# Optimization experiments

Hardware: AMD Instinct MI355X
Metric: run time of the kernel (lower is better)

The kernel has to match this reference:

```python
import jax, jax.numpy as jnp
import numpy as np

# FineMatching constants (from init_kwargs)
GRID_NUM = 8
VOXEL = 0.04
NDIM = 3
MAX_NEIGHBORS = 128
OFFSET = GRID_NUM * VOXEL / 2.0           # 0.16
RADIUS = (GRID_NUM + 1) * VOXEL / 2.0      # 0.18
G1 = GRID_NUM + 1                          # grid nodes per dim
G = G1 ** NDIM                             # 729 flattened voxel bins
NEG_BIG = -1e30


def setup_inputs() -> dict:
    key = jax.random.key(0)
    k1, k2, k3, k4, k5 = jax.random.split(key, 5)
    B, L0, L1, C = 4, 2048, 2048, 64
    x0 = jax.random.normal(k1, (B, L0, C), dtype=jnp.float32)
    x1 = jax.random.normal(k2, (B, L1, C), dtype=jnp.float32)
    pos0 = jax.random.uniform(k3, (B, L0, 3), dtype=jnp.float32)
    pos1 = jax.random.uniform(k4, (B, L1, 3), dtype=jnp.float32)
    pad_mask = jax.random.uniform(k5, (B, L1)) < 0.1  # True = padded / masked out
    return {"x0": x0, "x1": x1, "pos0": pos0, "pos1": pos1, "pad_mask": pad_mask}


def reference(x0, x1, pos0, pos1, pad_mask):
    B, L0, C = x0.shape
    K = MAX_NEIGHBORS
    # --- radius neighbor search (per batch, dense distances, K nearest) ---
    d2 = jnp.sum((pos0[:, :, None, :] - pos1[:, None, :, :]) ** 2, axis=-1)  # (B,L0,L1)
    neg_d2, idx = jax.lax.top_k(-d2, K)                                       # (B,L0,K)
    valid = (-neg_d2) < RADIUS ** 2                                           # within radius
    pad_g = jnp.take_along_axis(pad_mask[:, None, :], idx, axis=2)           # (B,L0,K)
    valid = valid & (~pad_g)
    # --- edge-wise gather + correlation ---
    x1g = jnp.take_along_axis(x1[:, None, :, :], idx[..., None], axis=2)     # (B,L0,K,C)
    corr = jnp.einsum('blc,blkc->blk', x0, x1g) / jnp.sqrt(jnp.float32(C))
    # --- masked segment softmax over neighbors (nan -> 0 when no valid edge) ---
    logits = jnp.where(valid, corr, NEG_BIG)
    prob = jax.nn.softmax(logits, axis=-1) * valid                            # (B,L0,K)
    # --- flow aggregation ---
    pos1g = jnp.take_along_axis(pos1[:, None, :, :], idx[..., None], axis=2) # (B,L0,K,3)
    dpos = pos1g - pos0[:, :, None, :]
    flow = jnp.einsum('blk,blkd->bld', prob, dpos)                            # (B,L0,3)
    # --- P2G voxel scatter: bin prob mass into (grid_num+1)^3 voxel grid ---
    coords = (dpos + OFFSET) / VOXEL
    vox = jnp.clip(jnp.round(coords), 0, GRID_NUM).astype(jnp.int32)          # (B,L0,K,3)
    flat = (vox[..., 0] * G1 + vox[..., 1]) * G1 + vox[..., 2]                # (B,L0,K)
    b_ix = jnp.arange(B)[:, None, None]
    l_ix = jnp.arange(L0)[None, :, None]
    flow_dist = jnp.zeros((B, L0, G), dtype=x0.dtype).at[b_ix, l_ix, flat].add(prob)
    return flow, flow_dist
```

## Files before the change

kernel.cpp:

```cpp
#include <hip/hip_runtime.h>
#include <stdint.h>

#define NB    4
#define NL0   2048
#define NL1   2048
#define NC    64
#define KMAX  128
#define CAP   256
#define NG1   9
#define NBINS 729
#define FLOWN (NB*NL0*3)
#define QPB   8
#define TPB   512

__global__ __launch_bounds__(TPB, 8) void fine_match_kernel(
    const float* __restrict__ x0, const float* __restrict__ x1,
    const float* __restrict__ pos0, const float* __restrict__ pos1,
    const void* __restrict__ padraw, float* __restrict__ out)
{
  __shared__ float          s_pos[NL1*3];
  __shared__ float          s_x0[QPB*NC];
  __shared__ float          s_p0[QPB][3];
  __shared__ unsigned short s_jj[QPB][CAP];
  __shared__ float          s_corr[QPB][CAP];

  const int t = threadIdx.x;
  const int bid = blockIdx.x;
  const int b = bid >> 8;
  const int l0base = (bid & 255) * QPB;

  int wide;
  {
    const uint32_t* pi = (const uint32_t*)padraw;
    int ok4 = 1;
    for (int i = t; i < (NB*NL1)/4; i += TPB) {
      const uint32_t v = pi[i];
      ok4 &= (int)((v <= 1u) | (v == 0x3F800000u));
    }
    wide = __syncthreads_and(ok4);
  }

  {
    const float4* src = (const float4*)(pos1 + (size_t)b*NL1*3);
    float4* dst = (float4*)s_pos;
    for (int i = t; i < NL1*3/4; i += TPB) dst[i] = src[i];
  }
  s_x0[t] = x0[(size_t)(b*NL0 + l0base)*NC + t];
  if (t < QPB*3) {
    const int q = t/3, c = t - q*3;
    s_p0[q][c] = pos0[(b*NL0 + l0base + q)*3 + c];
  }
  {
    float4 z4; z4.x = z4.y = z4.z = z4.w = 0.0f;
    float4* bz = (float4*)(out + FLOWN + (size_t)(b*NL0 + l0base)*NBINS);
    for (int i = t; i < QPB*NBINS/4; i += TPB) bz[i] = z4;
  }
  __syncthreads();

  const int wv = t >> 6, lane = t & 63;
  const int l0 = l0base + wv;
  const float p0x = s_p0[wv][0], p0y = s_p0[wv][1], p0z = s_p0[wv][2];

  int cnt = 0;
  for (int base = 0; base < NL1; base += 64) {
    const int j = base + lane;
    const float dx = __fsub_rn(s_pos[j*3+0], p0x);
    const float dy = __fsub_rn(s_pos[j*3+1], p0y);
    const float dz = __fsub_rn(s_pos[j*3+2], p0z);
    const float d2 = __fadd_rn(__fadd_rn(__fmul_rn(dx,dx), __fmul_rn(dy,dy)), __fmul_rn(dz,dz));
    const bool ok = d2 < 0.0324f;
    const uint64_t m = __ballot(ok);
    if (ok) {
      const int pos = cnt + (int)__popcll(m & ((1ull << lane) - 1ull));
      if (pos < CAP) s_jj[wv][pos] = (unsigned short)j;
    }
    cnt += (int)__popcll(m);
  }
  if (cnt > CAP) cnt = CAP;
  __syncthreads();

  const bool over = (cnt > KMAX);
  for (int s = 0; s < 4; ++s) {
    if (64*s >= cnt) break;
    const int i = lane + 64*s;
    if (i < cnt) {
      float c = -1e30f;
      const int j = (int)s_jj[wv][i];
      bool k;
      if (wide) k = (((const uint32_t*)padraw)[b*NL1 + j] == 0u);
      else      k = (((const uint8_t*)padraw)[b*NL1 + j] == 0);
      if (over && k) {
        const float dx = __fsub_rn(s_pos[j*3+0], p0x);
        const float dy = __fsub_rn(s_pos[j*3+1], p0y);
        const float dz = __fsub_rn(s_pos[j*3+2], p0z);
        const float di = __fadd_rn(__fadd_rn(__fmul_rn(dx,dx), __fmul_rn(dy,dy)), __fmul_rn(dz,dz));
        int rank = 0;
        for (int m2 = 0; m2 < cnt; ++m2) {
          const int jm = (int)s_jj[wv][m2];
          const float ex = __fsub_rn(s_pos[jm*3+0], p0x);
          const float ey = __fsub_rn(s_pos[jm*3+1], p0y);
          const float ez = __fsub_rn(s_pos[jm*3+2], p0z);
          const float dm = __fadd_rn(__fadd_rn(__fmul_rn(ex,ex), __fmul_rn(ey,ey)), __fmul_rn(ez,ez));
          rank += (dm < di || (dm == di && m2 < i)) ? 1 : 0;
        }
        if (rank >= KMAX) k = false;
      }
      if (k) {
        const float* xr = x1 + ((size_t)b*NL1 + j)*NC;
        float acc = 0.0f;
        #pragma unroll
        for (int cc = 0; cc < NC; cc += 4) {
          const float4 v = *(const float4*)(xr + cc);
          const float4 q = *(const float4*)(&s_x0[wv*NC + cc]);
          acc += q.x*v.x + q.y*v.y + q.z*v.z + q.w*v.w;
        }
        c = acc * 0.125f;
      }
      s_corr[wv][i] = c;
    }
  }

  float mx = -1e30f;
  for (int s = 0; s < 4; ++s) {
    if (64*s >= cnt) break;
    const int i = lane + 64*s;
    if (i < cnt) { const float c = s_corr[wv][i]; if (c > mx) mx = c; }
  }
  for (int off = 32; off; off >>= 1) { const float o = __shfl_xor(mx, off); if (o > mx) mx = o; }
  float sum = 0.0f;
  for (int s = 0; s < 4; ++s) {
    if (64*s >= cnt) break;
    const int i = lane + 64*s;
    if (i < cnt) { const float c = s_corr[wv][i]; if (c > -1e30f) sum += expf(c - mx); }
  }
  for (int off = 32; off; off >>= 1) sum += __shfl_xor(sum, off);
  const float inv = (sum > 0.0f) ? (1.0f / sum) : 0.0f;

  float* bins = out + FLOWN + (size_t)((size_t)b*NL0 + l0)*NBINS;
  float fx = 0.0f, fy = 0.0f, fz = 0.0f;
  for (int s = 0; s < 4; ++s) {
    if (64*s >= cnt) break;
    const int i = lane + 64*s;
    if (i < cnt) {
      const float c = s_corr[wv][i];
      if (c > -1e30f) {
        const float pv = expf(c - mx) * inv;
        const int j = (int)s_jj[wv][i];
        const float dx = __fsub_rn(s_pos[j*3+0], p0x);
        const float dy = __fsub_rn(s_pos[j*3+1], p0y);
        const float dz = __fsub_rn(s_pos[j*3+2], p0z);
        fx += pv*dx; fy += pv*dy; fz += pv*dz;
        const float cx = __fdiv_rn(__fadd_rn(dx, 0.16f), 0.04f);
        const float cy = __fdiv_rn(__fadd_rn(dy, 0.16f), 0.04f);
        const float cz = __fdiv_rn(__fadd_rn(dz, 0.16f), 0.04f);
        int vx = (int)rintf(cx); vx = vx < 0 ? 0 : (vx > 8 ? 8 : vx);
        int vy = (int)rintf(cy); vy = vy < 0 ? 0 : (vy > 8 ? 8 : vy);
        int vz = (int)rintf(cz); vz = vz < 0 ? 0 : (vz > 8 ? 8 : vz);
        __hip_atomic_fetch_add(&bins[(vx*NG1 + vy)*NG1 + vz], pv,
                               __ATOMIC_RELAXED, __HIP_MEMORY_SCOPE_WORKGROUP);
      }
    }
  }
  for (int off = 32; off; off >>= 1) {
    fx += __shfl_xor(fx, off); fy += __shfl_xor(fy, off); fz += __shfl_xor(fz, off);
  }
  if (lane == 0) {
    float* f = out + (size_t)((size_t)b*NL0 + l0)*3;
    f[0] = fx; f[1] = fy; f[2] = fz;
  }
}

extern "C" void kernel_launch(void* const* d_in, const int* in_sizes, int n_in,
                              void* d_out, int out_size, void* d_ws, size_t ws_size,
                              hipStream_t stream) {
  const float* x0   = (const float*)d_in[0];
  const float* x1   = (const float*)d_in[1];
  const float* pos0 = (const float*)d_in[2];
  const float* pos1 = (const float*)d_in[3];
  const void*  pad  = d_in[4];
  float* out = (float*)d_out;
  (void)in_sizes; (void)n_in; (void)out_size; (void)d_ws; (void)ws_size;
  hipLaunchKernelGGL(fine_match_kernel, dim3(NB*NL0/QPB), dim3(TPB), 0, stream,
                     x0, x1, pos0, pos1, pad, out);
}
```

Before: 29.63 us.

## Pack pos1 with pad flag into float4 LDS, double queries per block

Stores each pos1 point as a float4 in shared memory with the pad flag in the w component. Candidate filtering, ranking and binning then each need one LDS vector read instead of three scalar loads plus a global pad lookup. Blocks grow from 8 to 16 queries (1024 threads), which halves the number of times pos1 is restaged per batch. The output zeroing is moved ahead of the pad-format check so its stores are issued earlier. The larger block with the same launch bound may limit occupancy, and the pos1 staging now uses strided scalar global loads instead of float4 copies.

New measurement: 31.34 us. +5.8%, slower.

```diff
diff --git a/kernel.cpp b/kernel.cpp
--- a/kernel.cpp
+++ b/kernel.cpp
@@ -10,15 +10,15 @@
 #define NG1   9
 #define NBINS 729
 #define FLOWN (NB*NL0*3)
-#define QPB   8
-#define TPB   512
+#define QPB   16
+#define TPB   1024
 
 __global__ __launch_bounds__(TPB, 8) void fine_match_kernel(
     const float* __restrict__ x0, const float* __restrict__ x1,
     const float* __restrict__ pos0, const float* __restrict__ pos1,
     const void* __restrict__ padraw, float* __restrict__ out)
 {
-  __shared__ float          s_pos[NL1*3];
+  __shared__ float4         s_pos[NL1];
   __shared__ float          s_x0[QPB*NC];
   __shared__ float          s_p0[QPB][3];
   __shared__ unsigned short s_jj[QPB][CAP];
@@ -26,8 +26,14 @@
 
   const int t = threadIdx.x;
   const int bid = blockIdx.x;
-  const int b = bid >> 8;
-  const int l0base = (bid & 255) * QPB;
+  const int b = bid >> 7;
+  const int l0base = (bid & 127) * QPB;
+
+  {
+    float4 z4; z4.x = z4.y = z4.z = z4.w = 0.0f;
+    float4* bz = (float4*)(out + FLOWN + (size_t)(b*NL0 + l0base)*NBINS);
+    for (int i = t; i < QPB*NBINS/4; i += TPB) bz[i] = z4;
+  }
 
   int wide;
   {
@@ -41,19 +47,19 @@
   }
 
   {
-    const float4* src = (const float4*)(pos1 + (size_t)b*NL1*3);
-    float4* dst = (float4*)s_pos;
-    for (int i = t; i < NL1*3/4; i += TPB) dst[i] = src[i];
+    const float* p1b = pos1 + (size_t)b*NL1*3;
+    for (int i = t; i < NL1; i += TPB) {
+      float pv;
+      if (wide) pv = (((const uint32_t*)padraw)[b*NL1 + i] != 0u) ? 1.0f : 0.0f;
+      else      pv = (((const uint8_t*)padraw)[b*NL1 + i] != 0)   ? 1.0f : 0.0f;
+      float4 p; p.x = p1b[i*3+0]; p.y = p1b[i*3+1]; p.z = p1b[i*3+2]; p.w = pv;
+      s_pos[i] = p;
+    }
   }
   s_x0[t] = x0[(size_t)(b*NL0 + l0base)*NC + t];
   if (t < QPB*3) {
     const int q = t/3, c = t - q*3;
     s_p0[q][c] = pos0[(b*NL0 + l0base + q)*3 + c];
-  }
-  {
-    float4 z4; z4.x = z4.y = z4.z = z4.w = 0.0f;
-    float4* bz = (float4*)(out + FLOWN + (size_t)(b*NL0 + l0base)*NBINS);
-    for (int i = t; i < QPB*NBINS/4; i += TPB) bz[i] = z4;
   }
   __syncthreads();
 
@@ -64,9 +70,10 @@
   int cnt = 0;
   for (int base = 0; base < NL1; base += 64) {
     const int j = base + lane;
-    const float dx = __fsub_rn(s_pos[j*3+0], p0x);
-    const float dy = __fsub_rn(s_pos[j*3+1], p0y);
-    const float dz = __fsub_rn(s_pos[j*3+2], p0z);
+    const float4 p = s_pos[j];
+    const float dx = __fsub_rn(p.x, p0x);
+    const float dy = __fsub_rn(p.y, p0y);
+    const float dz = __fsub_rn(p.z, p0z);
     const float d2 = __fadd_rn(__fadd_rn(__fmul_rn(dx,dx), __fmul_rn(dy,dy)), __fmul_rn(dz,dz));
     const bool ok = d2 < 0.0324f;
     const uint64_t m = __ballot(ok);
@@ -86,20 +93,19 @@
     if (i < cnt) {
       float c = -1e30f;
       const int j = (int)s_jj[wv][i];
-      bool k;
-      if (wide) k = (((const uint32_t*)padraw)[b*NL1 + j] == 0u);
-      else      k = (((const uint8_t*)padraw)[b*NL1 + j] == 0);
+      const float4 pj = s_pos[j];
+      bool k = (pj.w == 0.0f);
       if (over && k) {
-        const float dx = __fsub_rn(s_pos[j*3+0], p0x);
-        const float dy = __fsub_rn(s_pos[j*3+1], p0y);
-        const float dz = __fsub_rn(s_pos[j*3+2], p0z);
+        const float dx = __fsub_rn(pj.x, p0x);
+        const float dy = __fsub_rn(pj.y, p0y);
+        const float dz = __fsub_rn(pj.z, p0z);
         const float di = __fadd_rn(__fadd_rn(__fmul_rn(dx,dx), __fmul_rn(dy,dy)), __fmul_rn(dz,dz));
         int rank = 0;
         for (int m2 = 0; m2 < cnt; ++m2) {
-          const int jm = (int)s_jj[wv][m2];
-          const float ex = __fsub_rn(s_pos[jm*3+0], p0x);
-          const float ey = __fsub_rn(s_pos[jm*3+1], p0y);
-          const float ez = __fsub_rn(s_pos[jm*3+2], p0z);
+          const float4 pm = s_pos[(int)s_jj[wv][m2]];
+          const float ex = __fsub_rn(pm.x, p0x);
+          const float ey = __fsub_rn(pm.y, p0y);
+          const float ez = __fsub_rn(pm.z, p0z);
           const float dm = __fadd_rn(__fadd_rn(__fmul_rn(ex,ex), __fmul_rn(ey,ey)), __fmul_rn(ez,ez));
           rank += (dm < di || (dm == di && m2 < i)) ? 1 : 0;
         }
@@ -145,10 +151,10 @@
       const float c = s_corr[wv][i];
       if (c > -1e30f) {
         const float pv = expf(c - mx) * inv;
-        const int j = (int)s_jj[wv][i];
-        const float dx = __fsub_rn(s_pos[j*3+0], p0x);
-        const float dy = __fsub_rn(s_pos[j*3+1], p0y);
-        const float dz = __fsub_rn(s_pos[j*3+2], p0z);
+        const float4 pj = s_pos[(int)s_jj[wv][i]];
+        const float dx = __fsub_rn(pj.x, p0x);
+        const float dy = __fsub_rn(pj.y, p0y);
+        const float dz = __fsub_rn(pj.z, p0z);
         fx += pv*dx; fy += pv*dy; fz += pv*dz;
         const float cx = __fdiv_rn(__fadd_rn(dx, 0.16f), 0.04f);
         const float cy = __fdiv_rn(__fadd_rn(dy, 0.16f), 0.04f);
```

## Process two queries per wave to reuse staged pos1 and halve block setup

Applied to the files above, without the earlier changes.

Doubles queries per block to 16, with each wave handling two queries. The candidate scan loads each pos1 point from LDS once and tests it against both queries, and the per-block pos1 staging and pad-format scan are amortized over twice as many queries. The trade-off is a halved grid and higher register pressure, with per-query softmax/scatter phases now serialized within a wave.

Result: slower. 30.92 us (+4.4%).

```diff
diff --git a/kernel.cpp b/kernel.cpp
--- a/kernel.cpp
+++ b/kernel.cpp
@@ -10,10 +10,10 @@
 #define NG1   9
 #define NBINS 729
 #define FLOWN (NB*NL0*3)
-#define QPB   8
+#define QPB   16
 #define TPB   512
 
-__global__ __launch_bounds__(TPB, 8) void fine_match_kernel(
+__global__ __launch_bounds__(TPB, 4) void fine_match_kernel(
     const float* __restrict__ x0, const float* __restrict__ x1,
     const float* __restrict__ pos0, const float* __restrict__ pos1,
     const void* __restrict__ padraw, float* __restrict__ out)
@@ -26,8 +26,8 @@
 
   const int t = threadIdx.x;
   const int bid = blockIdx.x;
-  const int b = bid >> 8;
-  const int l0base = (bid & 255) * QPB;
+  const int b = bid >> 7;
+  const int l0base = (bid & 127) * QPB;
 
   int wide;
   {
@@ -45,7 +45,8 @@
     float4* dst = (float4*)s_pos;
     for (int i = t; i < NL1*3/4; i += TPB) dst[i] = src[i];
   }
-  s_x0[t] = x0[(size_t)(b*NL0 + l0base)*NC + t];
+  for (int i = t; i < QPB*NC; i += TPB)
+    s_x0[i] = x0[(size_t)(b*NL0 + l0base)*NC + i];
   if (t < QPB*3) {
     const int q = t/3, c = t - q*3;
     s_p0[q][c] = pos0[(b*NL0 + l0base + q)*3 + c];
@@ -58,115 +59,135 @@
   __syncthreads();
 
   const int wv = t >> 6, lane = t & 63;
-  const int l0 = l0base + wv;
-  const float p0x = s_p0[wv][0], p0y = s_p0[wv][1], p0z = s_p0[wv][2];
-
-  int cnt = 0;
+  const int q0 = wv*2, q1 = wv*2 + 1;
+  const float ax = s_p0[q0][0], ay = s_p0[q0][1], az = s_p0[q0][2];
+  const float bx = s_p0[q1][0], by = s_p0[q1][1], bz = s_p0[q1][2];
+
+  int cnt0 = 0, cnt1 = 0;
   for (int base = 0; base < NL1; base += 64) {
     const int j = base + lane;
-    const float dx = __fsub_rn(s_pos[j*3+0], p0x);
-    const float dy = __fsub_rn(s_pos[j*3+1], p0y);
-    const float dz = __fsub_rn(s_pos[j*3+2], p0z);
-    const float d2 = __fadd_rn(__fadd_rn(__fmul_rn(dx,dx), __fmul_rn(dy,dy)), __fmul_rn(dz,dz));
-    const bool ok = d2 < 0.0324f;
-    const uint64_t m = __ballot(ok);
-    if (ok) {
-      const int pos = cnt + (int)__popcll(m & ((1ull << lane) - 1ull));
-      if (pos < CAP) s_jj[wv][pos] = (unsigned short)j;
-    }
-    cnt += (int)__popcll(m);
-  }
-  if (cnt > CAP) cnt = CAP;
-  __syncthreads();
-
-  const bool over = (cnt > KMAX);
-  for (int s = 0; s < 4; ++s) {
-    if (64*s >= cnt) break;
-    const int i = lane + 64*s;
-    if (i < cnt) {
-      float c = -1e30f;
-      const int j = (int)s_jj[wv][i];
-      bool k;
-      if (wide) k = (((const uint32_t*)padraw)[b*NL1 + j] == 0u);
-      else      k = (((const uint8_t*)padraw)[b*NL1 + j] == 0);
-      if (over && k) {
-        const float dx = __fsub_rn(s_pos[j*3+0], p0x);
-        const float dy = __fsub_rn(s_pos[j*3+1], p0y);
-        const float dz = __fsub_rn(s_pos[j*3+2], p0z);
-        const float di = __fadd_rn(__fadd_rn(__fmul_rn(dx,dx), __fmul_rn(dy,dy)), __fmul_rn(dz,dz));
-        int rank = 0;
-        for (int m2 = 0; m2 < cnt; ++m2) {
-          const int jm = (int)s_jj[wv][m2];
-          const float ex = __fsub_rn(s_pos[jm*3+0], p0x);
-          const float ey = __fsub_rn(s_pos[jm*3+1], p0y);
-          const float ez = __fsub_rn(s_pos[jm*3+2], p0z);
-          const float dm = __fadd_rn(__fadd_rn(__fmul_rn(ex,ex), __fmul_rn(ey,ey)), __fmul_rn(ez,ez));
-          rank += (dm < di || (dm == di && m2 < i)) ? 1 : 0;
+    const float px = s_pos[j*3+0], py = s_pos[j*3+1], pz = s_pos[j*3+2];
+    const float dxa = __fsub_rn(px, ax), dya = __fsub_rn(py, ay), dza = __fsub_rn(pz, az);
+    const float dxb = __fsub_rn(px, bx), dyb = __fsub_rn(py, by), dzb = __fsub_rn(pz, bz);
+    const float d2a = __fadd_rn(__fadd_rn(__fmul_rn(dxa,dxa), __fmul_rn(dya,dya)), __fmul_rn(dza,dza));
+    const float d2b = __fadd_rn(__fadd_rn(__fmul_rn(dxb,dxb), __fmul_rn(dyb,dyb)), __fmul_rn(dzb,dzb));
+    const bool oka = d2a < 0.0324f;
+    const bool okb = d2b < 0.0324f;
+    const uint64_t m0 = __ballot(oka);
+    const uint64_t m1 = __ballot(okb);
+    const uint64_t lm = (1ull << lane) - 1ull;
+    if (oka) {
+      const int pos = cnt0 + (int)__popcll(m0 & lm);
+      if (pos < CAP) s_jj[q0][pos] = (unsigned short)j;
+    }
+    if (okb) {
+      const int pos = cnt1 + (int)__popcll(m1 & lm);
+      if (pos < CAP) s_jj[q1][pos] = (unsigned short)j;
+    }
+    cnt0 += (int)__popcll(m0);
+    cnt1 += (int)__popcll(m1);
+  }
+  if (cnt0 > CAP) cnt0 = CAP;
+  if (cnt1 > CAP) cnt1 = CAP;
+
+  #pragma unroll
+  for (int u = 0; u < 2; ++u) {
+    const int qi  = (u == 0) ? q0 : q1;
+    const int cnt = (u == 0) ? cnt0 : cnt1;
+    const int l0  = l0base + qi;
+    const float p0x = (u == 0) ? ax : bx;
+    const float p0y = (u == 0) ? ay : by;
+    const float p0z = (u == 0) ? az : bz;
+
+    const bool over = (cnt > KMAX);
+    for (int s = 0; s < 4; ++s) {
+      if (64*s >= cnt) break;
+      const int i = lane + 64*s;
+      if (i < cnt) {
+        float c = -1e30f;
+        const int j = (int)s_jj[qi][i];
+        bool k;
+        if (wide) k = (((const uint32_t*)padraw)[b*NL1 + j] == 0u);
+        else      k = (((const uint8_t*)padraw)[b*NL1 + j] == 0);
+        if (over && k) {
+          const float dx = __fsub_rn(s_pos[j*3+0], p0x);
+          const float dy = __fsub_rn(s_pos[j*3+1], p0y);
+          const float dz = __fsub_rn(s_pos[j*3+2], p0z);
+          const float di = __fadd_rn(__fadd_rn(__fmul_rn(dx,dx), __fmul_rn(dy,dy)), __fmul_rn(dz,dz));
+          int rank = 0;
+          for (int m2 = 0; m2 < cnt; ++m2) {
+            const int jm = (int)s_jj[qi][m2];
+            const float ex = __fsub_rn(s_pos[jm*3+0], p0x);
+            const float ey = __fsub_rn(s_pos[jm*3+1], p0y);
+            const float ez = __fsub_rn(s_pos[jm*3+2], p0z);
+            const float dm = __fadd_rn(__fadd_rn(__fmul_rn(ex,ex), __fmul_rn(ey,ey)), __fmul_rn(ez,ez));
+            rank += (dm < di || (dm == di && m2 < i)) ? 1 : 0;
+          }
+          if (rank >= KMAX) k = false;
         }
-        if (rank >= KMAX) k = false;
+        if (k) {
+          const float* xr = x1 + ((size_t)b*NL1 + j)*NC;
+          float acc = 0.0f;
+          #pragma unroll
+          for (int cc = 0; cc < NC; cc += 4) {
+            const float4 v = *(const float4*)(xr + cc);
+            const float4 q = *(const float4*)(&s_x0[qi*NC + cc]);
+            acc += q.x*v.x + q.y*v.y + q.z*v.z + q.w*v.w;
+          }
+          c = acc * 0.125f;
+        }
+        s_corr[qi][i] = c;
       }
-      if (k) {
-        const float* xr = x1 + ((size_t)b*NL1 + j)*NC;
-        float acc = 0.0f;
-        #pragma unroll
-        for (int cc = 0; cc < NC; cc += 4) {
-          const float4 v = *(const float4*)(xr + cc);
-          const float4 q = *(const float4*)(&s_x0[wv*NC + cc]);
-          acc += q.x*v.x + q.y*v.y + q.z*v.z + q.w*v.w;
+    }
+
+    float mx = -1e30f;
+    for (int s = 0; s < 4; ++s) {
+      if (64*s >= cnt) break;
+      const int i = lane + 64*s;
+      if (i < cnt) { const float c = s_corr[qi][i]; if (c > mx) mx = c; }
+    }
+    for (int off = 32; off; off >>= 1) { const float o = __shfl_xor(mx, off); if (o > mx) mx = o; }
+    float sum = 0.0f;
+    for (int s = 0; s < 4; ++s) {
+      if (64*s >= cnt) break;
+      const int i = lane + 64*s;
+      if (i < cnt) { const float c = s_corr[qi][i]; if (c > -1e30f) sum += expf(c - mx); }
+    }
+    for (int off = 32; off; off >>= 1) sum += __shfl_xor(sum, off);
+    const float inv = (sum > 0.0f) ? (1.0f / sum) : 0.0f;
+
+    float* bins = out + FLOWN + (size_t)((size_t)b*NL0 + l0)*NBINS;
+    float fx = 0.0f, fy = 0.0f, fz = 0.0f;
+    for (int s = 0; s < 4; ++s) {
+      if (64*s >= cnt) break;
+      const int i = lane + 64*s;
+      if (i < cnt) {
+        const float c = s_corr[qi][i];
+        if (c > -1e30f) {
+          const float pv = expf(c - mx) * inv;
+          const int j = (int)s_jj[qi][i];
+          const float dx = __fsub_rn(s_pos[j*3+0], p0x);
+          const float dy = __fsub_rn(s_pos[j*3+1], p0y);
+          const float dz = __fsub_rn(s_pos[j*3+2], p0z);
+          fx += pv*dx; fy += pv*dy; fz += pv*dz;
+          const float cx = __fdiv_rn(__fadd_rn(dx, 0.16f), 0.04f);
+          const float cy = __fdiv_rn(__fadd_rn(dy, 0.16f), 0.04f);
+          const float cz = __fdiv_rn(__fadd_rn(dz, 0.16f), 0.04f);
+          int vx = (int)rintf(cx); vx = vx < 0 ? 0 : (vx > 8 ? 8 : vx);
+          int vy = (int)rintf(cy); vy = vy < 0 ? 0 : (vy > 8 ? 8 : vy);
+          int vz = (int)rintf(cz); vz = vz < 0 ? 0 : (vz > 8 ? 8 : vz);
+          __hip_atomic_fetch_add(&bins[(vx*NG1 + vy)*NG1 + vz], pv,
+                                 __ATOMIC_RELAXED, __HIP_MEMORY_SCOPE_WORKGROUP);
         }
-        c = acc * 0.125f;
       }
-      s_corr[wv][i] = c;
-    }
-  }
-
-  float mx = -1e30f;
-  for (int s = 0; s < 4; ++s) {
-    if (64*s >= cnt) break;
-    const int i = lane + 64*s;
-    if (i < cnt) { const float c = s_corr[wv][i]; if (c > mx) mx = c; }
-  }
-  for (int off = 32; off; off >>= 1) { const float o = __shfl_xor(mx, off); if (o > mx) mx = o; }
-  float sum = 0.0f;
-  for (int s = 0; s < 4; ++s) {
-    if (64*s >= cnt) break;
-    const int i = lane + 64*s;
-    if (i < cnt) { const float c = s_corr[wv][i]; if (c > -1e30f) sum += expf(c - mx); }
-  }
-  for (int off = 32; off; off >>= 1) sum += __shfl_xor(sum, off);
-  const float inv = (sum > 0.0f) ? (1.0f / sum) : 0.0f;
-
-  float* bins = out + FLOWN + (size_t)((size_t)b*NL0 + l0)*NBINS;
-  float fx = 0.0f, fy = 0.0f, fz = 0.0f;
-  for (int s = 0; s < 4; ++s) {
-    if (64*s >= cnt) break;
-    const int i = lane + 64*s;
-    if (i < cnt) {
-      const float c = s_corr[wv][i];
-      if (c > -1e30f) {
-        const float pv = expf(c - mx) * inv;
-        const int j = (int)s_jj[wv][i];
-        const float dx = __fsub_rn(s_pos[j*3+0], p0x);
-        const float dy = __fsub_rn(s_pos[j*3+1], p0y);
-        const float dz = __fsub_rn(s_pos[j*3+2], p0z);
-        fx += pv*dx; fy += pv*dy; fz += pv*dz;
-        const float cx = __fdiv_rn(__fadd_rn(dx, 0.16f), 0.04f);
-        const float cy = __fdiv_rn(__fadd_rn(dy, 0.16f), 0.04f);
-        const float cz = __fdiv_rn(__fadd_rn(dz, 0.16f), 0.04f);
-        int vx = (int)rintf(cx); vx = vx < 0 ? 0 : (vx > 8 ? 8 : vx);
-        int vy = (int)rintf(cy); vy = vy < 0 ? 0 : (vy > 8 ? 8 : vy);
-        int vz = (int)rintf(cz); vz = vz < 0 ? 0 : (vz > 8 ? 8 : vz);
-        __hip_atomic_fetch_add(&bins[(vx*NG1 + vy)*NG1 + vz], pv,
-                               __ATOMIC_RELAXED, __HIP_MEMORY_SCOPE_WORKGROUP);
-      }
-    }
-  }
-  for (int off = 32; off; off >>= 1) {
-    fx += __shfl_xor(fx, off); fy += __shfl_xor(fy, off); fz += __shfl_xor(fz, off);
-  }
-  if (lane == 0) {
-    float* f = out + (size_t)((size_t)b*NL0 + l0)*3;
-    f[0] = fx; f[1] = fy; f[2] = fz;
+    }
+    for (int off = 32; off; off >>= 1) {
+      fx += __shfl_xor(fx, off); fy += __shfl_xor(fy, off); fz += __shfl_xor(fz, off);
+    }
+    if (lane == 0) {
+      float* f = out + (size_t)((size_t)b*NL0 + l0)*3;
+      f[0] = fx; f[1] = fy; f[2] = fz;
+    }
   }
 }
 
```

## Accumulate voxel bins in LDS and keep correlations in registers

Applied to the files above, without the earlier changes.

Replaces the global zero-fill plus global atomics on the flow_dist histogram with a per-wave LDS histogram that is zeroed, filled with LDS atomics, and written once to global memory. Correlation scores move from shared memory into a small per-lane register array, and the candidate capacity drops from 256 to 192. This removes the separate zeroing pass and the global atomic traffic, at the cost of more LDS use per block (8x729 floats), which may reduce occupancy. Neighbourhoods with more than 192 in-radius points are now truncated, which can change results for dense inputs.

Result: slower. 35.15 us (+18.7%).

```diff
diff --git a/kernel.cpp b/kernel.cpp
--- a/kernel.cpp
+++ b/kernel.cpp
@@ -6,7 +6,8 @@
 #define NL1   2048
 #define NC    64
 #define KMAX  128
-#define CAP   256
+#define CAP   192
+#define NSLOT 3
 #define NG1   9
 #define NBINS 729
 #define FLOWN (NB*NL0*3)
@@ -22,7 +23,7 @@
   __shared__ float          s_x0[QPB*NC];
   __shared__ float          s_p0[QPB][3];
   __shared__ unsigned short s_jj[QPB][CAP];
-  __shared__ float          s_corr[QPB][CAP];
+  __shared__ float          s_bins[QPB][NBINS];
 
   const int t = threadIdx.x;
   const int bid = blockIdx.x;
@@ -50,16 +51,13 @@
     const int q = t/3, c = t - q*3;
     s_p0[q][c] = pos0[(b*NL0 + l0base + q)*3 + c];
   }
-  {
-    float4 z4; z4.x = z4.y = z4.z = z4.w = 0.0f;
-    float4* bz = (float4*)(out + FLOWN + (size_t)(b*NL0 + l0base)*NBINS);
-    for (int i = t; i < QPB*NBINS/4; i += TPB) bz[i] = z4;
-  }
   __syncthreads();
 
   const int wv = t >> 6, lane = t & 63;
   const int l0 = l0base + wv;
   const float p0x = s_p0[wv][0], p0y = s_p0[wv][1], p0z = s_p0[wv][2];
+
+  for (int i = lane; i < NBINS; i += 64) s_bins[wv][i] = 0.0f;
 
   int cnt = 0;
   for (int base = 0; base < NL1; base += 64) {
@@ -80,11 +78,14 @@
   __syncthreads();
 
   const bool over = (cnt > KMAX);
-  for (int s = 0; s < 4; ++s) {
+  float corr[NSLOT];
+  #pragma unroll
+  for (int s = 0; s < NSLOT; ++s) corr[s] = -1e30f;
+  #pragma unroll
+  for (int s = 0; s < NSLOT; ++s) {
     if (64*s >= cnt) break;
     const int i = lane + 64*s;
     if (i < cnt) {
-      float c = -1e30f;
       const int j = (int)s_jj[wv][i];
       bool k;
       if (wide) k = (((const uint32_t*)padraw)[b*NL1 + j] == 0u);
@@ -114,51 +115,40 @@
           const float4 q = *(const float4*)(&s_x0[wv*NC + cc]);
           acc += q.x*v.x + q.y*v.y + q.z*v.z + q.w*v.w;
         }
-        c = acc * 0.125f;
+        corr[s] = acc * 0.125f;
       }
-      s_corr[wv][i] = c;
     }
   }
 
   float mx = -1e30f;
-  for (int s = 0; s < 4; ++s) {
-    if (64*s >= cnt) break;
-    const int i = lane + 64*s;
-    if (i < cnt) { const float c = s_corr[wv][i]; if (c > mx) mx = c; }
-  }
+  #pragma unroll
+  for (int s = 0; s < NSLOT; ++s) if (corr[s] > mx) mx = corr[s];
   for (int off = 32; off; off >>= 1) { const float o = __shfl_xor(mx, off); if (o > mx) mx = o; }
   float sum = 0.0f;
-  for (int s = 0; s < 4; ++s) {
-    if (64*s >= cnt) break;
-    const int i = lane + 64*s;
-    if (i < cnt) { const float c = s_corr[wv][i]; if (c > -1e30f) sum += expf(c - mx); }
-  }
+  #pragma unroll
+  for (int s = 0; s < NSLOT; ++s) if (corr[s] > -1e30f) sum += expf(corr[s] - mx);
   for (int off = 32; off; off >>= 1) sum += __shfl_xor(sum, off);
   const float inv = (sum > 0.0f) ? (1.0f / sum) : 0.0f;
 
-  float* bins = out + FLOWN + (size_t)((size_t)b*NL0 + l0)*NBINS;
   float fx = 0.0f, fy = 0.0f, fz = 0.0f;
-  for (int s = 0; s < 4; ++s) {
+  #pragma unroll
+  for (int s = 0; s < NSLOT; ++s) {
     if (64*s >= cnt) break;
     const int i = lane + 64*s;
-    if (i < cnt) {
-      const float c = s_corr[wv][i];
-      if (c > -1e30f) {
-        const float pv = expf(c - mx) * inv;
-        const int j = (int)s_jj[wv][i];
-        const float dx = __fsub_rn(s_pos[j*3+0], p0x);
-        const float dy = __fsub_rn(s_pos[j*3+1], p0y);
-        const float dz = __fsub_rn(s_pos[j*3+2], p0z);
-        fx += pv*dx; fy += pv*dy; fz += pv*dz;
-        const float cx = __fdiv_rn(__fadd_rn(dx, 0.16f), 0.04f);
-        const float cy = __fdiv_rn(__fadd_rn(dy, 0.16f), 0.04f);
-        const float cz = __fdiv_rn(__fadd_rn(dz, 0.16f), 0.04f);
-        int vx = (int)rintf(cx); vx = vx < 0 ? 0 : (vx > 8 ? 8 : vx);
-        int vy = (int)rintf(cy); vy = vy < 0 ? 0 : (vy > 8 ? 8 : vy);
-        int vz = (int)rintf(cz); vz = vz < 0 ? 0 : (vz > 8 ? 8 : vz);
-        __hip_atomic_fetch_add(&bins[(vx*NG1 + vy)*NG1 + vz], pv,
-                               __ATOMIC_RELAXED, __HIP_MEMORY_SCOPE_WORKGROUP);
-      }
+    if (i < cnt && corr[s] > -1e30f) {
+      const float pv = expf(corr[s] - mx) * inv;
+      const int j = (int)s_jj[wv][i];
+      const float dx = __fsub_rn(s_pos[j*3+0], p0x);
+      const float dy = __fsub_rn(s_pos[j*3+1], p0y);
+      const float dz = __fsub_rn(s_pos[j*3+2], p0z);
+      fx += pv*dx; fy += pv*dy; fz += pv*dz;
+      const float cx = __fdiv_rn(__fadd_rn(dx, 0.16f), 0.04f);
+      const float cy = __fdiv_rn(__fadd_rn(dy, 0.16f), 0.04f);
+      const float cz = __fdiv_rn(__fadd_rn(dz, 0.16f), 0.04f);
+      int vx = (int)rintf(cx); vx = vx < 0 ? 0 : (vx > 8 ? 8 : vx);
+      int vy = (int)rintf(cy); vy = vy < 0 ? 0 : (vy > 8 ? 8 : vy);
+      int vz = (int)rintf(cz); vz = vz < 0 ? 0 : (vz > 8 ? 8 : vz);
+      atomicAdd(&s_bins[wv][(vx*NG1 + vy)*NG1 + vz], pv);
     }
   }
   for (int off = 32; off; off >>= 1) {
@@ -168,6 +158,9 @@
     float* f = out + (size_t)((size_t)b*NL0 + l0)*3;
     f[0] = fx; f[1] = fy; f[2] = fz;
   }
+
+  float* fd = out + FLOWN + (size_t)((size_t)b*NL0 + l0)*NBINS;
+  for (int i = lane; i < NBINS; i += 64) fd[i] = s_bins[wv][i];
 }
 
 extern "C" void kernel_launch(void* const* d_in, const int* in_sizes, int n_in,
```
